# Optimization experiments

Hardware: AMD Instinct MI355X
Metric: run time of the kernel (lower is better)

## Reference

```python
import jax, jax.numpy as jnp
import numpy as np
import math

B, NQ, NK = 8, 1024, 2048
DQ = DK = DV = 1024
H = 8
DH = DV // H
EPS = 1e-5


def _layernorm(x, g, b):
    mu = jnp.mean(x, axis=-1, keepdims=True)
    var = jnp.mean(jnp.square(x - mu), axis=-1, keepdims=True)
    return (x - mu) * jax.lax.rsqrt(var + EPS) * g + b


def setup_inputs() -> dict:
    key = jax.random.key(0)
    ks = jax.random.split(key, 12)
    s_q = 1.0 / math.sqrt(DQ)
    s_v = 1.0 / math.sqrt(DV)
    return {
        "Q": jax.random.normal(ks[0], (B, NQ, DQ), jnp.float32),
        "K": jax.random.normal(ks[1], (B, NK, DK), jnp.float32),
        "Wq": jax.random.normal(ks[2], (DQ, DV), jnp.float32) * s_q,
        "bq": jnp.zeros((DV,), jnp.float32),
        "Wk": jax.random.normal(ks[3], (DK, DV), jnp.float32) * s_q,
        "bk": jnp.zeros((DV,), jnp.float32),
        "Wv": jax.random.normal(ks[4], (DK, DV), jnp.float32) * s_q,
        "bv": jnp.zeros((DV,), jnp.float32),
        "Wo": jax.random.normal(ks[5], (DV, DV), jnp.float32) * s_v,
        "bo": jnp.zeros((DV,), jnp.float32),
        "g0": jnp.ones((DV,), jnp.float32),
        "b0": jnp.zeros((DV,), jnp.float32),
        "g1": jnp.ones((DV,), jnp.float32),
        "b1": jnp.zeros((DV,), jnp.float32),
    }


def reference(Q, K, Wq, bq, Wk, bk, Wv, bv, Wo, bo, g0, b0, g1, b1):
    # projections
    q = Q @ Wq + bq                      # [B, NQ, DV]
    k = K @ Wk + bk                      # [B, NK, DV]
    v = K @ Wv + bv                      # [B, NK, DV]
    qh = q.reshape(B, NQ, H, DH)
    kh = k.reshape(B, NK, H, DH)
    vh = v.reshape(B, NK, H, DH)
    # NOTE: original scales by sqrt(dim_V), not sqrt(d_head)
    scale = 1.0 / math.sqrt(DV)
    logits = jnp.einsum("bqhd,bkhd->bhqk", qh, kh) * scale
    A = jax.nn.softmax(logits, axis=-1)
    # residual baked into attention output: Q_ + A @ V_
    Oh = qh + jnp.einsum("bhqk,bkhd->bqhd", A, vh)
    O = Oh.reshape(B, NQ, DV)
    O = _layernorm(O, g0, b0)
    O = O + jax.nn.relu(O @ Wo + bo)
    O = _layernorm(O, g1, b1)
    return O
```

## Files before the change

kernel.cpp:

```cpp
#include <hip/hip_runtime.h>
#include <stdint.h>

#define DEVI static __device__ __forceinline__

typedef __attribute__((ext_vector_type(8))) short short8;
typedef __attribute__((ext_vector_type(4))) float floatx4;
typedef __attribute__((ext_vector_type(4))) unsigned short ushortx4;

DEVI unsigned short f2bf(float f) {
  union { float f; uint32_t u; } v; v.f = f;
  uint32_t r = v.u + 0x7FFFu + ((v.u >> 16) & 1u);
  return (unsigned short)(r >> 16);
}
DEVI float bf2f(unsigned short s) {
  union { uint32_t u; float f; } v; v.u = ((uint32_t)s) << 16;
  return v.f;
}
DEVI unsigned char f2fp8(float f) {
  return (unsigned char)(__builtin_amdgcn_cvt_pk_fp8_f32(f, f, 0, false) & 0xff);
}

DEVI void lds_cp16(void* lds, const void* g) {
  __builtin_amdgcn_global_load_lds(
      (const __attribute__((address_space(1))) uint32_t*)g,
      reinterpret_cast<__attribute__((address_space(3))) uint32_t*>(
          (uint32_t)reinterpret_cast<uintptr_t>(lds)),
      16, 0, 0);
}

__global__ __launch_bounds__(256) void cvt_qk(const float* __restrict__ Q,
                                              const float* __restrict__ K,
                                              unsigned short* __restrict__ Qb,
                                              unsigned char* __restrict__ Kf8) {
  const int bid = blockIdx.x;
  if (bid < 8192) {
    const size_t i = (size_t)bid * 256 + threadIdx.x;
    const floatx4 v = ((const floatx4*)Q)[i];
    ushortx4 o;
    o.x = f2bf(v.x); o.y = f2bf(v.y); o.z = f2bf(v.z); o.w = f2bf(v.w);
    ((ushortx4*)Qb)[i] = o;
  } else {
    const size_t i = (size_t)(bid - 8192) * 256 + threadIdx.x;
    const floatx4 v = ((const floatx4*)K)[i];
    int p = __builtin_amdgcn_cvt_pk_fp8_f32(v.x, v.y, 0, false);
    p = __builtin_amdgcn_cvt_pk_fp8_f32(v.z, v.w, p, true);
    ((int*)Kf8)[i] = p;
  }
}

__global__ __launch_bounds__(256) void wtrans4(const float* __restrict__ Wq,
                                               const float* __restrict__ Wk,
                                               const float* __restrict__ Wv,
                                               const float* __restrict__ Wo,
                                               unsigned short* __restrict__ Wt,
                                               unsigned char* __restrict__ Wt8) {
  __shared__ float t[32][33];
  const int tx = threadIdx.x, ty = threadIdx.y;
  const int z = blockIdx.z;
  const float* W = (z == 0) ? Wq : (z == 1) ? Wk : (z == 2) ? Wv : Wo;
  const int c0 = blockIdx.x * 32, r0 = blockIdx.y * 32;
#pragma unroll
  for (int i = 0; i < 4; i++)
    t[ty + i * 8][tx] = W[(size_t)(r0 + ty + i * 8) * 1024 + c0 + tx];
  __syncthreads();
  if (z == 0 || z == 3) {
    unsigned short* D = Wt + (z == 0 ? 0 : (size_t)1024 * 1024);
#pragma unroll
    for (int i = 0; i < 4; i++)
      D[(size_t)(c0 + ty + i * 8) * 1024 + r0 + tx] = f2bf(t[tx][ty + i * 8]);
  } else {
    unsigned char* D = Wt8 + (z == 1 ? 0 : (size_t)1024 * 1024);
#pragma unroll
    for (int i = 0; i < 4; i++)
      D[(size_t)(c0 + ty + i * 8) * 1024 + r0 + tx] = f2fp8(t[tx][ty + i * 8]);
  }
}

template <int EPI>
__global__ __launch_bounds__(256, 3) void gemm_bt(
    const unsigned short* __restrict__ A, const unsigned short* __restrict__ Bt,
    const float* __restrict__ bias, const unsigned short* __restrict__ X1,
    void* __restrict__ Cout) {
  __shared__ unsigned short As[2][4][128][8];
  __shared__ unsigned short Bs[2][4][128][8];

  const int tid = threadIdx.x;
  const int lane = tid & 63, w = tid >> 6;
  const int wr = w >> 1, wc = w & 1;
  const int qd = lane >> 4, l16 = lane & 15;
  const int bid = blockIdx.x;
  const int xcd = bid & 7, loc = bid >> 3;
  const int m0 = (xcd * 8 + (loc & 7)) * 128;
  const int n0 = (loc >> 3) * 128;

  floatx4 acc[4][4];
#pragma unroll
  for (int i = 0; i < 4; i++)
#pragma unroll
    for (int j = 0; j < 4; j++) { floatx4 z = {0.f, 0.f, 0.f, 0.f}; acc[i][j] = z; }

  const int prow = tid & 127;
  const unsigned short* aptr = A + (size_t)(m0 + prow) * 1024 + ((tid >> 7) << 3);
  const unsigned short* bptr = Bt + (size_t)(n0 + prow) * 1024 + ((tid >> 7) << 3);
  const int dstoff = tid * 8;

  lds_cp16(&As[0][0][0][0] + dstoff, aptr);
  lds_cp16(&As[0][0][0][0] + dstoff + 2048, aptr + 16);
  lds_cp16(&Bs[0][0][0][0] + dstoff, bptr);
  lds_cp16(&Bs[0][0][0][0] + dstoff + 2048, bptr + 16);

  for (int it = 0; it < 32; it++) {
    __syncthreads();
    if (it < 31) {
      const int nb = (it + 1) & 1, k0 = (it + 1) * 32;
      lds_cp16(&As[nb][0][0][0] + dstoff, aptr + k0);
      lds_cp16(&As[nb][0][0][0] + dstoff + 2048, aptr + k0 + 16);
      lds_cp16(&Bs[nb][0][0][0] + dstoff, bptr + k0);
      lds_cp16(&Bs[nb][0][0][0] + dstoff + 2048, bptr + k0 + 16);
    }
    const int cur = it & 1;
    short8 af[4], bf[4];
#pragma unroll
    for (int mi = 0; mi < 4; mi++)
      af[mi] = *(const short8*)&As[cur][qd][wr * 64 + mi * 16 + l16][0];
#pragma unroll
    for (int ni = 0; ni < 4; ni++)
      bf[ni] = *(const short8*)&Bs[cur][qd][wc * 64 + ni * 16 + l16][0];
#pragma unroll
    for (int mi = 0; mi < 4; mi++)
#pragma unroll
      for (int ni = 0; ni < 4; ni++)
        acc[mi][ni] =
            __builtin_amdgcn_mfma_f32_16x16x32_bf16(af[mi], bf[ni], acc[mi][ni], 0, 0, 0);
  }

#pragma unroll
  for (int mi = 0; mi < 4; mi++) {
#pragma unroll
    for (int ni = 0; ni < 4; ni++) {
      const int row = m0 + wr * 64 + mi * 16 + qd * 4;
      const int col = n0 + wc * 64 + ni * 16 + l16;
      const float bv = bias[col];
      if constexpr (EPI == 0) {
        unsigned short* C = (unsigned short*)Cout;
#pragma unroll
        for (int r = 0; r < 4; r++)
          C[(size_t)(row + r) * 1024 + col] = f2bf(acc[mi][ni][r] + bv);
      } else {
        float* C = (float*)Cout;
#pragma unroll
        for (int r = 0; r < 4; r++) {
          const float x1 = bf2f(X1[(size_t)(row + r) * 1024 + col]);
          C[(size_t)(row + r) * 1024 + col] = x1 + fmaxf(acc[mi][ni][r] + bv, 0.f);
        }
      }
    }
  }
}

__global__ __launch_bounds__(256, 3) void gemm_kv_f8(
    const unsigned char* __restrict__ A, const unsigned char* __restrict__ Bt,
    const float* __restrict__ biasK, const float* __restrict__ biasV,
    unsigned short* __restrict__ CK, unsigned short* __restrict__ CV) {
  __shared__ unsigned char As[2][4][128][16];
  __shared__ unsigned char Bs[2][4][128][16];

  const int tid = threadIdx.x;
  const int lane = tid & 63, w = tid >> 6;
  const int wr = w >> 1, wc = w & 1;
  const int qd = lane >> 4, l16 = lane & 15;
  const int bid = blockIdx.x;
  const int xcd = bid & 7, loc = bid >> 3;
  const int m0 = (xcd * 16 + (loc & 15)) * 128;
  const int n0 = (loc >> 4) * 128;

  floatx4 acc[4][4];
#pragma unroll
  for (int i = 0; i < 4; i++)
#pragma unroll
    for (int j = 0; j < 4; j++) { floatx4 z = {0.f, 0.f, 0.f, 0.f}; acc[i][j] = z; }

  const int srow = tid & 127, sc = tid >> 7;
  const unsigned char* aptr = A + (size_t)(m0 + srow) * 1024 + sc * 16;
  const unsigned char* bptr = Bt + (size_t)(n0 + srow) * 1024 + sc * 16;
  unsigned char* dA = &As[0][sc][srow][0];
  unsigned char* dB = &Bs[0][sc][srow][0];

  lds_cp16(dA, aptr);
  lds_cp16(dA + 4096, aptr + 32);
  lds_cp16(dB, bptr);
  lds_cp16(dB + 4096, bptr + 32);

  for (int it = 0; it < 16; it++) {
    __syncthreads();
    if (it < 15) {
      const int nb = (it + 1) & 1, k0 = (it + 1) * 64;
      lds_cp16(dA + nb * 8192, aptr + k0);
      lds_cp16(dA + nb * 8192 + 4096, aptr + k0 + 32);
      lds_cp16(dB + nb * 8192, bptr + k0);
      lds_cp16(dB + nb * 8192 + 4096, bptr + k0 + 32);
    }
    const int cur = it & 1;
    const int coff = (qd & 1) * 8, chi = qd >> 1;
    long a8[4][2], b8[4][2];
#pragma unroll
    for (int mi = 0; mi < 4; mi++) {
      const int row = wr * 64 + mi * 16 + l16;
      a8[mi][0] = *(const long*)&As[cur][chi][row][coff];
      a8[mi][1] = *(const long*)&As[cur][2 + chi][row][coff];
    }
#pragma unroll
    for (int ni = 0; ni < 4; ni++) {
      const int row = wc * 64 + ni * 16 + l16;
      b8[ni][0] = *(const long*)&Bs[cur][chi][row][coff];
      b8[ni][1] = *(const long*)&Bs[cur][2 + chi][row][coff];
    }
#pragma unroll
    for (int mi = 0; mi < 4; mi++)
#pragma unroll
      for (int ni = 0; ni < 4; ni++)
        acc[mi][ni] = __builtin_amdgcn_mfma_f32_16x16x32_fp8_fp8(
            a8[mi][0], b8[ni][0], acc[mi][ni], 0, 0, 0);
#pragma unroll
    for (int mi = 0; mi < 4; mi++)
#pragma unroll
      for (int ni = 0; ni < 4; ni++)
        acc[mi][ni] = __builtin_amdgcn_mfma_f32_16x16x32_fp8_fp8(
            a8[mi][1], b8[ni][1], acc[mi][ni], 0, 0, 0);
  }

#pragma unroll
  for (int mi = 0; mi < 4; mi++) {
#pragma unroll
    for (int ni = 0; ni < 4; ni++) {
      const int row = m0 + wr * 64 + mi * 16 + qd * 4;
      const int col = n0 + wc * 64 + ni * 16 + l16;
      if (col < 1024) {
        const float bv = biasK[col];
#pragma unroll
        for (int r = 0; r < 4; r++)
          CK[(size_t)(row + r) * 1024 + col] = f2bf(acc[mi][ni][r] + bv);
      } else {
        const int vc = col - 1024;
        const float bv = biasV[vc];
        const int bb = row >> 11, nk = row & 2047;
        const int hh = vc >> 7, dh = vc & 127;
        ushortx4 pk;
        pk.x = f2bf(acc[mi][ni][0] + bv);
        pk.y = f2bf(acc[mi][ni][1] + bv);
        pk.z = f2bf(acc[mi][ni][2] + bv);
        pk.w = f2bf(acc[mi][ni][3] + bv);
        *(ushortx4*)&CV[(size_t)((bb * 8 + hh) * 128 + dh) * 2048 + nk] = pk;
      }
    }
  }
}

__global__ __launch_bounds__(256, 2) void attn(
    const unsigned short* __restrict__ qb, const unsigned short* __restrict__ kb,
    const unsigned short* __restrict__ vt, unsigned short* __restrict__ Ob) {
  __shared__ unsigned short smem[32768];

  const int tid = threadIdx.x;
  const int lane = tid & 63, w = tid >> 6;
  const int qd = lane >> 4, l16 = lane & 15;
  const int bid = blockIdx.x;
  const int qt = bid >> 6, bh = bid & 63;
  const int h = bh >> 3, b = bh & 7;
  const int m0 = qt * 128;

  const size_t qbase = ((size_t)(b * 1024 + m0)) * 1024 + h * 128;
  const size_t kbase = ((size_t)(b * 2048)) * 1024 + h * 128;
  const size_t vbase = ((size_t)((b * 8 + h) * 128)) * 2048;

#pragma unroll
  for (int i = 0; i < 8; i++) {
    const int p = i * 256 + tid;
    const int row = p & 127, c = p >> 7;
    lds_cp16(&smem[c * 1024 + row * 8], qb + qbase + (size_t)row * 1024 + c * 8);
  }
#pragma unroll
  for (int i = 0; i < 2; i++) {
    const int p = i * 256 + tid;
    const int kr = p & 31, kc = p >> 5;
    lds_cp16(&smem[16384 + kc * 256 + kr * 8], kb + kbase + (size_t)kr * 1024 + kc * 8);
    const int dh = p & 127, vc = p >> 7;
    lds_cp16(&smem[24576 + vc * 1024 + dh * 8], vt + vbase + (size_t)dh * 2048 + vc * 8);
  }
  __syncthreads();

  short8 qf[2][4];
#pragma unroll
  for (int mi = 0; mi < 2; mi++)
#pragma unroll
    for (int ks = 0; ks < 4; ks++)
      qf[mi][ks] =
          *(const short8*)&smem[(ks * 4 + qd) * 1024 + ((w * 2 + mi) * 16 + l16) * 8];
  __syncthreads();

  floatx4 oacc[2][8];
#pragma unroll
  for (int mi = 0; mi < 2; mi++)
#pragma unroll
    for (int ni = 0; ni < 8; ni++) { floatx4 z = {0.f, 0.f, 0.f, 0.f}; oacc[mi][ni] = z; }
  float lsum[2][4];
#pragma unroll
  for (int mi = 0; mi < 2; mi++)
#pragma unroll
    for (int r = 0; r < 4; r++) lsum[mi][r] = 0.f;

  for (int it = 0; it < 64; it++) {
    if (it) __syncthreads();
    if (it + 1 < 64) {
      const int nb = (it + 1) & 1, kv0 = (it + 1) * 32;
#pragma unroll
      for (int i = 0; i < 2; i++) {
        const int p = i * 256 + tid;
        const int kr = p & 31, kc = p >> 5;
        lds_cp16(&smem[16384 + nb * 4096 + kc * 256 + kr * 8],
                 kb + kbase + (size_t)(kv0 + kr) * 1024 + kc * 8);
        const int dh = p & 127, vc = p >> 7;
        lds_cp16(&smem[24576 + nb * 4096 + vc * 1024 + dh * 8],
                 vt + vbase + (size_t)dh * 2048 + kv0 + vc * 8);
      }
    }
    const int cur = it & 1;

    floatx4 sacc[2][2];
#pragma unroll
    for (int mi = 0; mi < 2; mi++)
#pragma unroll
      for (int ni = 0; ni < 2; ni++) { floatx4 z = {0.f, 0.f, 0.f, 0.f}; sacc[mi][ni] = z; }
#pragma unroll
    for (int ks = 0; ks < 4; ks++) {
      short8 b0 = *(const short8*)&smem[16384 + cur * 4096 + (ks * 4 + qd) * 256 + l16 * 8];
      short8 b1 =
          *(const short8*)&smem[16384 + cur * 4096 + (ks * 4 + qd) * 256 + (16 + l16) * 8];
#pragma unroll
      for (int mi = 0; mi < 2; mi++) {
        sacc[mi][0] = __builtin_amdgcn_mfma_f32_16x16x32_bf16(qf[mi][ks], b0, sacc[mi][0], 0, 0, 0);
        sacc[mi][1] = __builtin_amdgcn_mfma_f32_16x16x32_bf16(qf[mi][ks], b1, sacc[mi][1], 0, 0, 0);
      }
    }

#pragma unroll
    for (int mi = 0; mi < 2; mi++)
#pragma unroll
      for (int ni = 0; ni < 2; ni++) {
        const int kvl = ni * 16 + l16;
#pragma unroll
        for (int r = 0; r < 4; r++) {
          const float e = __expf(sacc[mi][ni][r] * 0.03125f);
          lsum[mi][r] += e;
          smem[(kvl >> 3) * 1024 + ((w * 2 + mi) * 16 + qd * 4 + r) * 8 + (kvl & 7)] = f2bf(e);
        }
      }

    short8 pf[2];
#pragma unroll
    for (int mi = 0; mi < 2; mi++)
      pf[mi] = *(const short8*)&smem[qd * 1024 + ((w * 2 + mi) * 16 + l16) * 8];
#pragma unroll
    for (int ni = 0; ni < 8; ni++) {
      const short8 vf = *(const short8*)&smem[24576 + cur * 4096 + qd * 1024 + (ni * 16 + l16) * 8];
#pragma unroll
      for (int mi = 0; mi < 2; mi++)
        oacc[mi][ni] = __builtin_amdgcn_mfma_f32_16x16x32_bf16(pf[mi], vf, oacc[mi][ni], 0, 0, 0);
    }
  }

  float inv[2][4];
#pragma unroll
  for (int mi = 0; mi < 2; mi++)
#pragma unroll
    for (int r = 0; r < 4; r++) {
      float s = lsum[mi][r];
      s += __shfl_xor(s, 1); s += __shfl_xor(s, 2);
      s += __shfl_xor(s, 4); s += __shfl_xor(s, 8);
      inv[mi][r] = 1.f / s;
    }

#pragma unroll
  for (int mi = 0; mi < 2; mi++)
#pragma unroll
    for (int ni = 0; ni < 8; ni++)
#pragma unroll
      for (int r = 0; r < 4; r++) {
        const int m = (w * 2 + mi) * 16 + qd * 4 + r;
        const int dh = ni * 16 + l16;
        const float qv = bf2f(qb[qbase + (size_t)m * 1024 + dh]);
        Ob[qbase + (size_t)m * 1024 + dh] = f2bf(qv + oacc[mi][ni][r] * inv[mi][r]);
      }
}

__global__ __launch_bounds__(256) void ln_rows(const unsigned short* __restrict__ X,
                                               const float* __restrict__ g,
                                               const float* __restrict__ bb,
                                               unsigned short* __restrict__ Y) {
  __shared__ float red[8];
  const int row = blockIdx.x, tid = threadIdx.x;
  const int w = tid >> 6, lane = tid & 63;
  const ushortx4 u = ((const ushortx4*)(X + (size_t)row * 1024))[tid];
  float x0 = bf2f(u.x), x1 = bf2f(u.y), x2 = bf2f(u.z), x3 = bf2f(u.w);
  float s = x0 + x1 + x2 + x3;
  float s2 = x0 * x0 + x1 * x1 + x2 * x2 + x3 * x3;
#pragma unroll
  for (int off = 1; off < 64; off <<= 1) { s += __shfl_xor(s, off); s2 += __shfl_xor(s2, off); }
  if (lane == 0) { red[w] = s; red[4 + w] = s2; }
  __syncthreads();
  s = red[0] + red[1] + red[2] + red[3];
  s2 = red[4] + red[5] + red[6] + red[7];
  const float mu = s * (1.f / 1024.f);
  const float rs = rsqrtf(s2 * (1.f / 1024.f) - mu * mu + 1e-5f);
  const floatx4 gv = ((const floatx4*)g)[tid];
  const floatx4 bv = ((const floatx4*)bb)[tid];
  ushortx4 o;
  o.x = f2bf((x0 - mu) * rs * gv.x + bv.x);
  o.y = f2bf((x1 - mu) * rs * gv.y + bv.y);
  o.z = f2bf((x2 - mu) * rs * gv.z + bv.z);
  o.w = f2bf((x3 - mu) * rs * gv.w + bv.w);
  ((ushortx4*)(Y + (size_t)row * 1024))[tid] = o;
}

__global__ __launch_bounds__(256) void ln_f32(const float* __restrict__ X,
                                              const float* __restrict__ g,
                                              const float* __restrict__ bb,
                                              float* __restrict__ out) {
  __shared__ float red[8];
  const int row = blockIdx.x, tid = threadIdx.x;
  const int w = tid >> 6, lane = tid & 63;
  const floatx4 xv = ((const floatx4*)(X + (size_t)row * 1024))[tid];
  float x0 = xv.x, x1 = xv.y, x2 = xv.z, x3 = xv.w;
  float s = x0 + x1 + x2 + x3;
  float s2 = x0 * x0 + x1 * x1 + x2 * x2 + x3 * x3;
#pragma unroll
  for (int off = 1; off < 64; off <<= 1) { s += __shfl_xor(s, off); s2 += __shfl_xor(s2, off); }
  if (lane == 0) { red[w] = s; red[4 + w] = s2; }
  __syncthreads();
  s = red[0] + red[1] + red[2] + red[3];
  s2 = red[4] + red[5] + red[6] + red[7];
  const float mu = s * (1.f / 1024.f);
  const float rs = rsqrtf(s2 * (1.f / 1024.f) - mu * mu + 1e-5f);
  const floatx4 gv = ((const floatx4*)g)[tid];
  const floatx4 bv = ((const floatx4*)bb)[tid];
  floatx4 o;
  o.x = (x0 - mu) * rs * gv.x + bv.x;
  o.y = (x1 - mu) * rs * gv.y + bv.y;
  o.z = (x2 - mu) * rs * gv.z + bv.z;
  o.w = (x3 - mu) * rs * gv.w + bv.w;
  ((floatx4*)(out + (size_t)row * 1024))[tid] = o;
}

extern "C" void kernel_launch(void* const* d_in, const int* in_sizes, int n_in,
                              void* d_out, int out_size, void* d_ws, size_t ws_size,
                              hipStream_t stream) {
  (void)in_sizes; (void)n_in; (void)out_size; (void)ws_size;
  const float* Q  = (const float*)d_in[0];
  const float* K  = (const float*)d_in[1];
  const float* Wq = (const float*)d_in[2];
  const float* bq = (const float*)d_in[3];
  const float* Wk = (const float*)d_in[4];
  const float* bk = (const float*)d_in[5];
  const float* Wv = (const float*)d_in[6];
  const float* bv = (const float*)d_in[7];
  const float* Wo = (const float*)d_in[8];
  const float* bo = (const float*)d_in[9];
  const float* g0 = (const float*)d_in[10];
  const float* b0 = (const float*)d_in[11];
  const float* g1 = (const float*)d_in[12];
  const float* b1 = (const float*)d_in[13];
  float* out = (float*)d_out;

  char* ws = (char*)d_ws;
  const size_t MB = 1u << 20;
  unsigned short* Qb  = (unsigned short*)(ws + 0);
  unsigned short* X1  = (unsigned short*)(ws + 16 * MB);
  unsigned short* Wt  = (unsigned short*)(ws + 32 * MB);
  unsigned char*  Wt8 = (unsigned char*)(ws + 36 * MB);
  unsigned char*  Kf8 = (unsigned char*)(ws + 38 * MB);
  unsigned short* qbp = (unsigned short*)(ws + 54 * MB);
  unsigned short* kbp = (unsigned short*)(ws + 70 * MB);
  unsigned short* vtp = (unsigned short*)(ws + 102 * MB);
  unsigned short* O   = Qb;
  float* O2 = (float*)(ws + 70 * MB);

  unsigned short* Wqt = Wt;
  unsigned short* Wot = Wt + (size_t)1024 * 1024;

  cvt_qk<<<24576, 256, 0, stream>>>(Q, K, Qb, Kf8);
  wtrans4<<<dim3(32, 32, 4), dim3(32, 8), 0, stream>>>(Wq, Wk, Wv, Wo, Wt, Wt8);

  gemm_bt<0><<<512, 256, 0, stream>>>(Qb, Wqt, bq, nullptr, qbp);
  gemm_kv_f8<<<2048, 256, 0, stream>>>(Kf8, Wt8, bk, bv, kbp, vtp);
  attn<<<512, 256, 0, stream>>>(qbp, kbp, vtp, O);
  ln_rows<<<8192, 256, 0, stream>>>(O, g0, b0, X1);
  gemm_bt<2><<<512, 256, 0, stream>>>(X1, Wot, bo, X1, O2);
  ln_f32<<<8192, 256, 0, stream>>>(O2, g1, b1, out);
}
```

Before: 437.9 us.

## Transpose attention MFMA so softmax probs stay in registers via bpermute

```diff
diff --git a/kernel.cpp b/kernel.cpp
--- a/kernel.cpp
+++ b/kernel.cpp
@@ -12,9 +12,17 @@
   uint32_t r = v.u + 0x7FFFu + ((v.u >> 16) & 1u);
   return (unsigned short)(r >> 16);
 }
+DEVI unsigned short f2bf_trunc(float f) {
+  union { float f; uint32_t u; } v; v.f = f;
+  return (unsigned short)(v.u >> 16);
+}
 DEVI float bf2f(unsigned short s) {
   union { uint32_t u; float f; } v; v.u = ((uint32_t)s) << 16;
   return v.f;
+}
+DEVI uint32_t fbits(float f) {
+  union { float f; uint32_t u; } v; v.f = f;
+  return v.u;
 }
 DEVI unsigned char f2fp8(float f) {
   return (unsigned char)(__builtin_amdgcn_cvt_pk_fp8_f32(f, f, 0, false) & 0xff);
@@ -256,10 +264,10 @@
   }
 }
 
-__global__ __launch_bounds__(256, 2) void attn(
+__global__ __launch_bounds__(256, 3) void attn(
     const unsigned short* __restrict__ qb, const unsigned short* __restrict__ kb,
     const unsigned short* __restrict__ vt, unsigned short* __restrict__ Ob) {
-  __shared__ unsigned short smem[32768];
+  __shared__ unsigned short smem[16384];
 
   const int tid = threadIdx.x;
   const int lane = tid & 63, w = tid >> 6;
@@ -279,118 +287,144 @@
     const int row = p & 127, c = p >> 7;
     lds_cp16(&smem[c * 1024 + row * 8], qb + qbase + (size_t)row * 1024 + c * 8);
   }
+  __syncthreads();
+  short8 qf[2][4];
+#pragma unroll
+  for (int nt = 0; nt < 2; nt++)
+#pragma unroll
+    for (int ks = 0; ks < 4; ks++)
+      qf[nt][ks] =
+          *(const short8*)&smem[(ks * 4 + qd) * 1024 + (w * 32 + nt * 16 + l16) * 8];
+  __syncthreads();
+
 #pragma unroll
   for (int i = 0; i < 2; i++) {
     const int p = i * 256 + tid;
     const int kr = p & 31, kc = p >> 5;
-    lds_cp16(&smem[16384 + kc * 256 + kr * 8], kb + kbase + (size_t)kr * 1024 + kc * 8);
+    lds_cp16(&smem[kc * 256 + kr * 8], kb + kbase + (size_t)kr * 1024 + kc * 8);
     const int dh = p & 127, vc = p >> 7;
-    lds_cp16(&smem[24576 + vc * 1024 + dh * 8], vt + vbase + (size_t)dh * 2048 + vc * 8);
-  }
-  __syncthreads();
-
-  short8 qf[2][4];
-#pragma unroll
-  for (int mi = 0; mi < 2; mi++)
-#pragma unroll
-    for (int ks = 0; ks < 4; ks++)
-      qf[mi][ks] =
-          *(const short8*)&smem[(ks * 4 + qd) * 1024 + ((w * 2 + mi) * 16 + l16) * 8];
-  __syncthreads();
-
-  floatx4 oacc[2][8];
-#pragma unroll
-  for (int mi = 0; mi < 2; mi++)
-#pragma unroll
-    for (int ni = 0; ni < 8; ni++) { floatx4 z = {0.f, 0.f, 0.f, 0.f}; oacc[mi][ni] = z; }
-  float lsum[2][4];
-#pragma unroll
-  for (int mi = 0; mi < 2; mi++)
-#pragma unroll
-    for (int r = 0; r < 4; r++) lsum[mi][r] = 0.f;
+    lds_cp16(&smem[8192 + vc * 1024 + dh * 8], vt + vbase + (size_t)dh * 2048 + vc * 8);
+  }
+
+  floatx4 oacc[8][2];
+#pragma unroll
+  for (int mt = 0; mt < 8; mt++)
+#pragma unroll
+    for (int nt = 0; nt < 2; nt++) { floatx4 z = {0.f, 0.f, 0.f, 0.f}; oacc[mt][nt] = z; }
+  float lsum[2] = {0.f, 0.f};
+
+  const int addrLo = ((qd & 1) * 32 + l16) * 4;
+  const int addrHi = addrLo + 64;
+  const bool loHalf = (lane < 32);
 
   for (int it = 0; it < 64; it++) {
-    if (it) __syncthreads();
+    __syncthreads();
     if (it + 1 < 64) {
       const int nb = (it + 1) & 1, kv0 = (it + 1) * 32;
 #pragma unroll
       for (int i = 0; i < 2; i++) {
         const int p = i * 256 + tid;
         const int kr = p & 31, kc = p >> 5;
-        lds_cp16(&smem[16384 + nb * 4096 + kc * 256 + kr * 8],
+        lds_cp16(&smem[nb * 4096 + kc * 256 + kr * 8],
                  kb + kbase + (size_t)(kv0 + kr) * 1024 + kc * 8);
         const int dh = p & 127, vc = p >> 7;
-        lds_cp16(&smem[24576 + nb * 4096 + vc * 1024 + dh * 8],
+        lds_cp16(&smem[8192 + nb * 4096 + vc * 1024 + dh * 8],
                  vt + vbase + (size_t)dh * 2048 + kv0 + vc * 8);
       }
     }
     const int cur = it & 1;
 
-    floatx4 sacc[2][2];
-#pragma unroll
-    for (int mi = 0; mi < 2; mi++)
-#pragma unroll
-      for (int ni = 0; ni < 2; ni++) { floatx4 z = {0.f, 0.f, 0.f, 0.f}; sacc[mi][ni] = z; }
+    floatx4 st[2][2];
+#pragma unroll
+    for (int mt = 0; mt < 2; mt++)
+#pragma unroll
+      for (int nt = 0; nt < 2; nt++) { floatx4 z = {0.f, 0.f, 0.f, 0.f}; st[mt][nt] = z; }
 #pragma unroll
     for (int ks = 0; ks < 4; ks++) {
-      short8 b0 = *(const short8*)&smem[16384 + cur * 4096 + (ks * 4 + qd) * 256 + l16 * 8];
-      short8 b1 =
-          *(const short8*)&smem[16384 + cur * 4096 + (ks * 4 + qd) * 256 + (16 + l16) * 8];
-#pragma unroll
-      for (int mi = 0; mi < 2; mi++) {
-        sacc[mi][0] = __builtin_amdgcn_mfma_f32_16x16x32_bf16(qf[mi][ks], b0, sacc[mi][0], 0, 0, 0);
-        sacc[mi][1] = __builtin_amdgcn_mfma_f32_16x16x32_bf16(qf[mi][ks], b1, sacc[mi][1], 0, 0, 0);
-      }
-    }
-
-#pragma unroll
-    for (int mi = 0; mi < 2; mi++)
-#pragma unroll
-      for (int ni = 0; ni < 2; ni++) {
-        const int kvl = ni * 16 + l16;
-#pragma unroll
-        for (int r = 0; r < 4; r++) {
-          const float e = __expf(sacc[mi][ni][r] * 0.03125f);
-          lsum[mi][r] += e;
-          smem[(kvl >> 3) * 1024 + ((w * 2 + mi) * 16 + qd * 4 + r) * 8 + (kvl & 7)] = f2bf(e);
-        }
-      }
-
-    short8 pf[2];
-#pragma unroll
-    for (int mi = 0; mi < 2; mi++)
-      pf[mi] = *(const short8*)&smem[qd * 1024 + ((w * 2 + mi) * 16 + l16) * 8];
-#pragma unroll
-    for (int ni = 0; ni < 8; ni++) {
-      const short8 vf = *(const short8*)&smem[24576 + cur * 4096 + qd * 1024 + (ni * 16 + l16) * 8];
-#pragma unroll
-      for (int mi = 0; mi < 2; mi++)
-        oacc[mi][ni] = __builtin_amdgcn_mfma_f32_16x16x32_bf16(pf[mi], vf, oacc[mi][ni], 0, 0, 0);
-    }
-  }
-
-  float inv[2][4];
-#pragma unroll
-  for (int mi = 0; mi < 2; mi++)
-#pragma unroll
-    for (int r = 0; r < 4; r++) {
-      float s = lsum[mi][r];
-      s += __shfl_xor(s, 1); s += __shfl_xor(s, 2);
-      s += __shfl_xor(s, 4); s += __shfl_xor(s, 8);
-      inv[mi][r] = 1.f / s;
-    }
-
-#pragma unroll
-  for (int mi = 0; mi < 2; mi++)
-#pragma unroll
-    for (int ni = 0; ni < 8; ni++)
+      const short8 ka = *(const short8*)&smem[cur * 4096 + (ks * 4 + qd) * 256 + l16 * 8];
+      const short8 kb2 =
+          *(const short8*)&smem[cur * 4096 + (ks * 4 + qd) * 256 + (16 + l16) * 8];
+#pragma unroll
+      for (int nt = 0; nt < 2; nt++) {
+        st[0][nt] = __builtin_amdgcn_mfma_f32_16x16x32_bf16(ka, qf[nt][ks], st[0][nt], 0, 0, 0);
+        st[1][nt] = __builtin_amdgcn_mfma_f32_16x16x32_bf16(kb2, qf[nt][ks], st[1][nt], 0, 0, 0);
+      }
+    }
+
+    uint32_t pk[2][2][2];
+#pragma unroll
+    for (int mt = 0; mt < 2; mt++)
+#pragma unroll
+      for (int nt = 0; nt < 2; nt++) {
+        const float e0 = __expf(st[mt][nt][0] * 0.03125f);
+        const float e1 = __expf(st[mt][nt][1] * 0.03125f);
+        const float e2 = __expf(st[mt][nt][2] * 0.03125f);
+        const float e3 = __expf(st[mt][nt][3] * 0.03125f);
+        lsum[nt] += (e0 + e1) + (e2 + e3);
+        pk[mt][nt][0] = __builtin_amdgcn_perm(fbits(e1), fbits(e0), 0x07060302);
+        pk[mt][nt][1] = __builtin_amdgcn_perm(fbits(e3), fbits(e2), 0x07060302);
+      }
+
+#pragma unroll
+    for (int nt = 0; nt < 2; nt++) {
+      int d0a = __builtin_amdgcn_ds_bpermute(addrLo, (int)pk[0][nt][0]);
+      int d0b = __builtin_amdgcn_ds_bpermute(addrLo, (int)pk[1][nt][0]);
+      int d1a = __builtin_amdgcn_ds_bpermute(addrLo, (int)pk[0][nt][1]);
+      int d1b = __builtin_amdgcn_ds_bpermute(addrLo, (int)pk[1][nt][1]);
+      int d2a = __builtin_amdgcn_ds_bpermute(addrHi, (int)pk[0][nt][0]);
+      int d2b = __builtin_amdgcn_ds_bpermute(addrHi, (int)pk[1][nt][0]);
+      int d3a = __builtin_amdgcn_ds_bpermute(addrHi, (int)pk[0][nt][1]);
+      int d3b = __builtin_amdgcn_ds_bpermute(addrHi, (int)pk[1][nt][1]);
+      union { int i[4]; short8 s; } u;
+      u.i[0] = loHalf ? d0a : d0b;
+      u.i[1] = loHalf ? d1a : d1b;
+      u.i[2] = loHalf ? d2a : d2b;
+      u.i[3] = loHalf ? d3a : d3b;
+      const short8 pf = u.s;
+#pragma unroll
+      for (int mt = 0; mt < 8; mt++) {
+        const short8 vf =
+            *(const short8*)&smem[8192 + cur * 4096 + qd * 1024 + (mt * 16 + l16) * 8];
+        oacc[mt][nt] = __builtin_amdgcn_mfma_f32_16x16x32_bf16(vf, pf, oacc[mt][nt], 0, 0, 0);
+      }
+    }
+  }
+
+  float inv[2];
+#pragma unroll
+  for (int nt = 0; nt < 2; nt++) {
+    float s = lsum[nt];
+    s += __shfl_xor(s, 16);
+    s += __shfl_xor(s, 32);
+    inv[nt] = 1.f / s;
+  }
+
+  __syncthreads();
+#pragma unroll
+  for (int mt = 0; mt < 8; mt++)
+#pragma unroll
+    for (int nt = 0; nt < 2; nt++) {
+      const int q = w * 32 + nt * 16 + l16;
 #pragma unroll
       for (int r = 0; r < 4; r++) {
-        const int m = (w * 2 + mi) * 16 + qd * 4 + r;
-        const int dh = ni * 16 + l16;
-        const float qv = bf2f(qb[qbase + (size_t)m * 1024 + dh]);
-        Ob[qbase + (size_t)m * 1024 + dh] = f2bf(qv + oacc[mi][ni][r] * inv[mi][r]);
-      }
+        const int dh = mt * 16 + qd * 4 + r;
+        const int c = dh >> 3, off = dh & 7;
+        smem[q * 128 + ((c ^ (q & 15)) * 8) + off] = f2bf_trunc(oacc[mt][nt][r] * inv[nt]);
+      }
+    }
+  __syncthreads();
+#pragma unroll
+  for (int i = 0; i < 8; i++) {
+    const int p = i * 256 + tid;
+    const int row = p >> 4, c = p & 15;
+    const short8 ov = *(const short8*)&smem[row * 128 + ((c ^ (row & 15)) * 8)];
+    const short8 qres = *(const short8*)(qb + qbase + (size_t)row * 1024 + c * 8);
+    union { unsigned short us[8]; short8 s; } o;
+#pragma unroll
+    for (int e = 0; e < 8; e++)
+      o.us[e] = f2bf(bf2f((unsigned short)ov[e]) + bf2f((unsigned short)qres[e]));
+    *(short8*)(Ob + qbase + (size_t)row * 1024 + c * 8) = o.s;
+  }
 }
 
 __global__ __launch_bounds__(256) void ln_rows(const unsigned short* __restrict__ X,
```

After: 430.9 us. No clear change (-1.6%).
